# Performance work log

Measured on AMD Instinct MI355X. Metric: run time of the kernel, lower is better.

Reference implementation:

```python
import jax, jax.numpy as jnp
import numpy as np

S = 3          # n_latent_split
H = 12         # hidden_size
W_SPLIT = 6    # latents.shape[1] // S  (18 W+ layers / 3 splits)
L = 512        # StyleGAN latent dim
N_NOISE = 4
R = 4          # fixed gaussian blur radius (jit-able stand-in for int(4*sigma))


def _gauss_smooth(n, sigma):
    """Per-sample variable-sigma Gaussian blur along the time axis.
    n: [B,T,s,s], sigma: [B] -> [B,T,s,s]"""
    sigma = jnp.maximum(sigma, 1e-3)
    k = jnp.arange(-R, R + 1, dtype=jnp.float32)            # [K]
    w = jnp.exp(-0.5 * (k[None, :] ** 2) / (sigma[:, None] ** 2))  # [B,K]
    w = w / w.sum(axis=1, keepdims=True)
    T = n.shape[1]
    npad = jnp.pad(n, ((0, 0), (R, R), (0, 0), (0, 0)), mode='reflect')
    out = jnp.zeros_like(n)
    for j in range(2 * R + 1):  # fixed tiny kernel-tap loop
        out = out + w[:, j, None, None, None] * npad[:, j:j + T]
    return out


def setup_inputs() -> dict:
    key = jax.random.key(0)
    ks = jax.random.split(key, 6)
    B, T = 8, 2048
    x = jax.random.uniform(ks[0], (B, T, S * H + 3 * N_NOISE), dtype=jnp.float32)
    latents_table = jax.random.normal(ks[1], (S * H, S * W_SPLIT, L), dtype=jnp.float32)
    inp = {"x": x, "latents_table": latents_table}
    for i in range(N_NOISE):
        size = 2 ** (i + 2)
        inp[f"eps_{i}"] = jax.random.normal(ks[2 + i], (B, T, size, size), dtype=jnp.float32)
    return inp


def reference(x, latents_table, eps_0, eps_1, eps_2, eps_3):
    # --- latent mixing branch ---
    lat_parts = []
    for i in range(S):
        env = x[..., i * H:(i + 1) * H]                              # [B,T,H]
        lat = latents_table[i * H:(i + 1) * H, i * W_SPLIT:(i + 1) * W_SPLIT, :]  # [H,W,L]
        lat_parts.append(jnp.einsum('bth,hwl->btwl', env, lat))
    lats = jnp.concatenate(lat_parts, axis=2)                        # [B,T,S*W,L]
    lats = lats - lats.mean(axis=1, keepdims=True)

    # --- noise branch ---
    noise_envs = x[..., S * H:]                                      # [B,T,3*N_NOISE]
    eps = [eps_0, eps_1, eps_2, eps_3]
    noises = []
    for i in range(N_NOISE):
        mu = noise_envs[..., 3 * i][..., None, None]
        sig = noise_envs[..., 3 * i + 1][..., None, None]
        smooth = noise_envs[..., 3 * i + 2]                          # [B,T]
        n = mu + sig * eps[i]                                        # [B,T,s,s]
        n = _gauss_smooth(n, smooth.mean(axis=1))
        noises.append(n)
    return (lats, *noises)
```

## Files before the change

kernel.cpp:

```cpp
#include <hip/hip_runtime.h>
#include <cstddef>

#define C_X   48
#define NB    8
#define NT    2048
#define TT    64

typedef float f32x4 __attribute__((ext_vector_type(4)));

__global__ __launch_bounds__(64) void means_kernel(const float* __restrict__ x,
                                                   float* __restrict__ means,
                                                   int T) {
    int bc = blockIdx.x;
    int b = bc / C_X, c = bc % C_X;
    float s = 0.f;
    for (int t = threadIdx.x; t < T; t += 64)
        s += x[((size_t)b * T + t) * C_X + c];
    #pragma unroll
    for (int off = 32; off > 0; off >>= 1)
        s += __shfl_down(s, off);
    if (threadIdx.x == 0) means[bc] = s / (float)T;
}

__global__ __launch_bounds__(128) void lats_kernel(const float* __restrict__ x,
                                                   const float* __restrict__ table,
                                                   const float* __restrict__ means,
                                                   float* __restrict__ out,
                                                   int T) {
    const int b  = blockIdx.x;
    const int w  = blockIdx.y;
    const int tc = blockIdx.z;
    const int i  = w / 6;
    const int wl = w % 6;
    const int tid = threadIdx.x;
    const int l  = tid * 4;

    float4 tab[12];
    #pragma unroll
    for (int h = 0; h < 12; ++h)
        tab[h] = *(const float4*)&table[(((size_t)(i * 12 + h) * 18) + (i * 6 + wl)) * 512 + l];

    __shared__ float env_s[TT][12];
    for (int idx = tid; idx < TT * 12; idx += 128) {
        int tt = idx / 12, h = idx % 12;
        int t  = tc * TT + tt;
        env_s[tt][h] = x[((size_t)(b * T + t)) * C_X + i * 12 + h]
                     - means[b * C_X + i * 12 + h];
    }
    __syncthreads();

    size_t obase = (((size_t)(b * T + tc * TT)) * 18 + w) * 512 + l;
    const size_t ostride = (size_t)18 * 512;
    for (int tt = 0; tt < TT; ++tt) {
        float4 e0 = *(const float4*)&env_s[tt][0];
        float4 e1 = *(const float4*)&env_s[tt][4];
        float4 e2 = *(const float4*)&env_s[tt][8];
        float e[12] = {e0.x, e0.y, e0.z, e0.w,
                       e1.x, e1.y, e1.z, e1.w,
                       e2.x, e2.y, e2.z, e2.w};
        f32x4 acc = {0.f, 0.f, 0.f, 0.f};
        #pragma unroll
        for (int h = 0; h < 12; ++h) {
            acc.x += e[h] * tab[h].x;
            acc.y += e[h] * tab[h].y;
            acc.z += e[h] * tab[h].z;
            acc.w += e[h] * tab[h].w;
        }
        __builtin_nontemporal_store(acc, (f32x4*)&out[obase + (size_t)tt * ostride]);
    }
}

__global__ __launch_bounds__(256) void noise_kernel(const float* __restrict__ x,
                                                    const float* __restrict__ eps,
                                                    const float* __restrict__ means,
                                                    float* __restrict__ out,
                                                    int T, int P, int PP, int TC,
                                                    int ch_base) {
    const int tid   = threadIdx.x;
    const int pp    = tid % PP;
    const int lane  = tid / PP;
    const int lanes = blockDim.x / PP;
    const int b     = blockIdx.x;
    const int p     = blockIdx.y * PP + pp;
    const int t0    = (blockIdx.z * lanes + lane) * TC;

    float sigma = fmaxf(means[b * C_X + ch_base + 2], 0.001f);
    float inv2s2 = -0.5f / (sigma * sigma);
    float w[9];
    float wsum = 0.f;
    #pragma unroll
    for (int j = 0; j < 9; ++j) {
        float k = (float)(j - 4);
        w[j] = expf(k * k * inv2s2);
        wsum += w[j];
    }
    float winv = 1.0f / wsum;
    #pragma unroll
    for (int j = 0; j < 9; ++j) w[j] *= winv;

    auto raw = [&](int tt) -> float {
        if (tt < 0)  tt = -tt;
        if (tt >= T) tt = 2 * T - 2 - tt;
        size_t row = (size_t)(b * T + tt);
        float mu = x[row * C_X + ch_base];
        float sg = x[row * C_X + ch_base + 1];
        float ep = __builtin_nontemporal_load(&eps[row * (size_t)P + p]);
        return mu + sg * ep;
    };

    float win[9];
    #pragma unroll
    for (int j = 0; j < 8; ++j) win[j + 1] = raw(t0 - 4 + j);

    for (int t = t0; t < t0 + TC; ++t) {
        #pragma unroll
        for (int j = 0; j < 8; ++j) win[j] = win[j + 1];
        win[8] = raw(t + 4);
        float acc = 0.f;
        #pragma unroll
        for (int j = 0; j < 9; ++j) acc += w[j] * win[j];
        __builtin_nontemporal_store(acc, &out[(size_t)(b * T + t) * P + p]);
    }
}

extern "C" void kernel_launch(void* const* d_in, const int* in_sizes, int n_in,
                              void* d_out, int out_size, void* d_ws, size_t ws_size,
                              hipStream_t stream) {
    const float* x     = (const float*)d_in[0];
    const float* table = (const float*)d_in[1];
    const float* epss[4] = {(const float*)d_in[2], (const float*)d_in[3],
                            (const float*)d_in[4], (const float*)d_in[5]};
    float* out   = (float*)d_out;
    float* means = (float*)d_ws;

    const int B = NB, T = NT;

    means_kernel<<<B * C_X, 64, 0, stream>>>(x, means, T);

    dim3 gl(B, 18, T / TT);
    lats_kernel<<<gl, 128, 0, stream>>>(x, table, means, out, T);

    size_t off = (size_t)B * T * 18 * 512;
    const int Ps[4]  = {16, 64, 256, 1024};
    const int PPs[4] = {16, 64, 256, 256};
    const int TCs[4] = {8, 32, 64, 64};
    for (int i = 0; i < 4; ++i) {
        int P = Ps[i], PP = PPs[i], TC = TCs[i];
        int lanes = 256 / PP;
        dim3 gn(B, P / PP, T / (lanes * TC));
        noise_kernel<<<gn, 256, 0, stream>>>(x, epss[i], means, out + off,
                                             T, P, PP, TC, 36 + 3 * i);
        off += (size_t)B * T * P;
    }
}
```

Before: 837.8 us.

## Fuse latent mixing and four noise blurs into one vectorized mega kernel

Replaces the separate lats kernel and four noise kernel launches with a single kernel that splits its flat block index between latent-mixing work and each noise level. Latent blocks now use 256 threads covering 128 time steps, with the two thread halves taking separate time ranges. Noise threads now process four pixels each using float4 loads and stores, and block counts and TC are retuned. The aim is to cut launch overhead and tail idle time and to widen memory accesses. The cost is more complex indexing and register pressure from the float4 blur windows.

```diff
diff --git a/kernel.cpp b/kernel.cpp
--- a/kernel.cpp
+++ b/kernel.cpp
@@ -4,7 +4,7 @@
 #define C_X   48
 #define NB    8
 #define NT    2048
-#define TT    64
+#define TTL   128
 
 typedef float f32x4 __attribute__((ext_vector_type(4)));
 
@@ -22,67 +22,94 @@
     if (threadIdx.x == 0) means[bc] = s / (float)T;
 }
 
-__global__ __launch_bounds__(128) void lats_kernel(const float* __restrict__ x,
+__global__ __launch_bounds__(256) void mega_kernel(const float* __restrict__ x,
                                                    const float* __restrict__ table,
                                                    const float* __restrict__ means,
+                                                   const float* __restrict__ eps0,
+                                                   const float* __restrict__ eps1,
+                                                   const float* __restrict__ eps2,
+                                                   const float* __restrict__ eps3,
                                                    float* __restrict__ out,
                                                    int T) {
-    const int b  = blockIdx.x;
-    const int w  = blockIdx.y;
-    const int tc = blockIdx.z;
-    const int i  = w / 6;
-    const int wl = w % 6;
     const int tid = threadIdx.x;
-    const int l  = tid * 4;
+    int bid = blockIdx.x;
+    const int TCHUNKS = T / TTL;
+    const int LATS_BLOCKS = NB * 18 * TCHUNKS;
 
-    float4 tab[12];
-    #pragma unroll
-    for (int h = 0; h < 12; ++h)
-        tab[h] = *(const float4*)&table[(((size_t)(i * 12 + h) * 18) + (i * 6 + wl)) * 512 + l];
+    if (bid < LATS_BLOCKS) {
+        const int tc = bid % TCHUNKS;
+        const int b  = (bid / TCHUNKS) % NB;
+        const int w  = bid / (TCHUNKS * NB);
+        const int i  = w / 6;
+        const int wl = w % 6;
+        const int l4 = tid & 127;
+        const int th = tid >> 7;
+        const int l  = l4 * 4;
 
-    __shared__ float env_s[TT][12];
-    for (int idx = tid; idx < TT * 12; idx += 128) {
-        int tt = idx / 12, h = idx % 12;
-        int t  = tc * TT + tt;
-        env_s[tt][h] = x[((size_t)(b * T + t)) * C_X + i * 12 + h]
-                     - means[b * C_X + i * 12 + h];
+        float4 tab[12];
+        #pragma unroll
+        for (int h = 0; h < 12; ++h)
+            tab[h] = *(const float4*)&table[(((size_t)(i * 12 + h) * 18) + (i * 6 + wl)) * 512 + l];
+
+        __shared__ float env_s[TTL][12];
+        for (int idx = tid; idx < TTL * 12; idx += 256) {
+            int tt = idx / 12, h = idx % 12;
+            int t  = tc * TTL + tt;
+            env_s[tt][h] = x[((size_t)(b * T + t)) * C_X + i * 12 + h]
+                         - means[b * C_X + i * 12 + h];
+        }
+        __syncthreads();
+
+        const int tt0 = th * (TTL / 2);
+        size_t obase = (((size_t)(b * T + tc * TTL + tt0)) * 18 + w) * 512 + l;
+        const size_t ostride = (size_t)18 * 512;
+        for (int tt = tt0; tt < tt0 + TTL / 2; ++tt) {
+            float4 e0 = *(const float4*)&env_s[tt][0];
+            float4 e1 = *(const float4*)&env_s[tt][4];
+            float4 e2 = *(const float4*)&env_s[tt][8];
+            float e[12] = {e0.x, e0.y, e0.z, e0.w,
+                           e1.x, e1.y, e1.z, e1.w,
+                           e2.x, e2.y, e2.z, e2.w};
+            f32x4 acc = {0.f, 0.f, 0.f, 0.f};
+            #pragma unroll
+            for (int h = 0; h < 12; ++h) {
+                acc.x += e[h] * tab[h].x;
+                acc.y += e[h] * tab[h].y;
+                acc.z += e[h] * tab[h].z;
+                acc.w += e[h] * tab[h].w;
+            }
+            __builtin_nontemporal_store(acc, (f32x4*)&out[obase]);
+            obase += ostride;
+        }
+        return;
     }
-    __syncthreads();
 
-    size_t obase = (((size_t)(b * T + tc * TT)) * 18 + w) * 512 + l;
-    const size_t ostride = (size_t)18 * 512;
-    for (int tt = 0; tt < TT; ++tt) {
-        float4 e0 = *(const float4*)&env_s[tt][0];
-        float4 e1 = *(const float4*)&env_s[tt][4];
-        float4 e2 = *(const float4*)&env_s[tt][8];
-        float e[12] = {e0.x, e0.y, e0.z, e0.w,
-                       e1.x, e1.y, e1.z, e1.w,
-                       e2.x, e2.y, e2.z, e2.w};
-        f32x4 acc = {0.f, 0.f, 0.f, 0.f};
-        #pragma unroll
-        for (int h = 0; h < 12; ++h) {
-            acc.x += e[h] * tab[h].x;
-            acc.y += e[h] * tab[h].y;
-            acc.z += e[h] * tab[h].z;
-            acc.w += e[h] * tab[h].w;
-        }
-        __builtin_nontemporal_store(acc, (f32x4*)&out[obase + (size_t)tt * ostride]);
+    bid -= LATS_BLOCKS;
+    const float* eps; int P, PPv, TC, ch_base; size_t ooff;
+    const size_t noise_base = (size_t)NB * T * 18 * 512;
+    if (bid < 32) {
+        eps = eps0; P = 16;   PPv = 4;   TC = 8;  ch_base = 36;
+        ooff = noise_base;
+    } else if (bid < 96) {
+        bid -= 32;
+        eps = eps1; P = 64;   PPv = 16;  TC = 16; ch_base = 39;
+        ooff = noise_base + (size_t)NB * T * 16;
+    } else if (bid < 224) {
+        bid -= 96;
+        eps = eps2; P = 256;  PPv = 64;  TC = 32; ch_base = 42;
+        ooff = noise_base + (size_t)NB * T * 80;
+    } else {
+        bid -= 224;
+        eps = eps3; P = 1024; PPv = 256; TC = 32; ch_base = 45;
+        ooff = noise_base + (size_t)NB * T * 336;
     }
-}
-
-__global__ __launch_bounds__(256) void noise_kernel(const float* __restrict__ x,
-                                                    const float* __restrict__ eps,
-                                                    const float* __restrict__ means,
-                                                    float* __restrict__ out,
-                                                    int T, int P, int PP, int TC,
-                                                    int ch_base) {
-    const int tid   = threadIdx.x;
-    const int pp    = tid % PP;
-    const int lane  = tid / PP;
-    const int lanes = blockDim.x / PP;
-    const int b     = blockIdx.x;
-    const int p     = blockIdx.y * PP + pp;
-    const int t0    = (blockIdx.z * lanes + lane) * TC;
+    const int b    = bid % NB;
+    const int gz   = bid / NB;
+    const int pp   = tid % PPv;
+    const int lane = tid / PPv;
+    const int lanes = 256 / PPv;
+    const int t0   = (gz * lanes + lane) * TC;
+    const int p0   = pp * 4;
 
     float sigma = fmaxf(means[b * C_X + ch_base + 2], 0.001f);
     float inv2s2 = -0.5f / (sigma * sigma);
@@ -98,28 +125,28 @@
     #pragma unroll
     for (int j = 0; j < 9; ++j) w[j] *= winv;
 
-    auto raw = [&](int tt) -> float {
+    auto raw4 = [&](int tt) -> f32x4 {
         if (tt < 0)  tt = -tt;
         if (tt >= T) tt = 2 * T - 2 - tt;
         size_t row = (size_t)(b * T + tt);
         float mu = x[row * C_X + ch_base];
         float sg = x[row * C_X + ch_base + 1];
-        float ep = __builtin_nontemporal_load(&eps[row * (size_t)P + p]);
-        return mu + sg * ep;
+        f32x4 e = __builtin_nontemporal_load((const f32x4*)&eps[row * (size_t)P + p0]);
+        return mu + sg * e;
     };
 
-    float win[9];
+    f32x4 win[9];
     #pragma unroll
-    for (int j = 0; j < 8; ++j) win[j + 1] = raw(t0 - 4 + j);
+    for (int j = 0; j < 8; ++j) win[j + 1] = raw4(t0 - 4 + j);
 
     for (int t = t0; t < t0 + TC; ++t) {
         #pragma unroll
         for (int j = 0; j < 8; ++j) win[j] = win[j + 1];
-        win[8] = raw(t + 4);
-        float acc = 0.f;
+        win[8] = raw4(t + 4);
+        f32x4 acc = w[0] * win[0];
         #pragma unroll
-        for (int j = 0; j < 9; ++j) acc += w[j] * win[j];
-        __builtin_nontemporal_store(acc, &out[(size_t)(b * T + t) * P + p]);
+        for (int j = 1; j < 9; ++j) acc += w[j] * win[j];
+        __builtin_nontemporal_store(acc, (f32x4*)&out[ooff + (size_t)(b * T + t) * P + p0]);
     }
 }
 
@@ -128,8 +155,6 @@
                               hipStream_t stream) {
     const float* x     = (const float*)d_in[0];
     const float* table = (const float*)d_in[1];
-    const float* epss[4] = {(const float*)d_in[2], (const float*)d_in[3],
-                            (const float*)d_in[4], (const float*)d_in[5]};
     float* out   = (float*)d_out;
     float* means = (float*)d_ws;
 
@@ -137,19 +162,10 @@
 
     means_kernel<<<B * C_X, 64, 0, stream>>>(x, means, T);
 
-    dim3 gl(B, 18, T / TT);
-    lats_kernel<<<gl, 128, 0, stream>>>(x, table, means, out, T);
-
-    size_t off = (size_t)B * T * 18 * 512;
-    const int Ps[4]  = {16, 64, 256, 1024};
-    const int PPs[4] = {16, 64, 256, 256};
-    const int TCs[4] = {8, 32, 64, 64};
-    for (int i = 0; i < 4; ++i) {
-        int P = Ps[i], PP = PPs[i], TC = TCs[i];
-        int lanes = 256 / PP;
-        dim3 gn(B, P / PP, T / (lanes * TC));
-        noise_kernel<<<gn, 256, 0, stream>>>(x, epss[i], means, out + off,
-                                             T, P, PP, TC, 36 + 3 * i);
-        off += (size_t)B * T * P;
-    }
+    const int TCHUNKS = T / TTL;
+    const int nblk = B * 18 * TCHUNKS + 736;
+    mega_kernel<<<nblk, 256, 0, stream>>>(x, table, means,
+                                          (const float*)d_in[2], (const float*)d_in[3],
+                                          (const float*)d_in[4], (const float*)d_in[5],
+                                          out, T);
 }
```

After: 775.8 us. 1.08x faster.
